# Optimization experiments

Measured on AMD Instinct MI355X. Metric: run time of the kernel, lower is better.

Reference implementation:

```python
import jax, jax.numpy as jnp
import numpy as np

# Supernet configuration (matches init_kwargs)
HIDDEN = [1024, 2048]
HEADS = [8, 16]
ABITS = [4, 8]
WBITS = [4, 8]
B, S = 4, 4096
MAX_IN = max(HIDDEN)            # 2048
MAX_OUT = max(HIDDEN)           # min(heads)*max(hidden)//min(heads) = 2048


def fake_quant(v, s, bit):
    """LSQ-style symmetric fake quantization with straight-through rounding."""
    qp = float(2 ** (bit - 1) - 1)
    qn = -float(2 ** (bit - 1))
    vs = jnp.clip(v / s, qn, qp)
    vq = vs + jax.lax.stop_gradient(jnp.round(vs) - vs)  # STE round
    return vq * s


def setup_inputs() -> dict:
    key = jax.random.key(0)
    k1, k2, k3, k4 = jax.random.split(key, 4)
    x = jax.random.normal(k1, (B, S, MAX_IN), jnp.float32)
    weights = jax.random.uniform(k2, (16,), jnp.float32)  # arch mixing coeffs
    W = jax.random.normal(k3, (MAX_OUT, MAX_IN), jnp.float32) * 0.02
    b = jax.random.normal(k4, (MAX_OUT,), jnp.float32) * 0.02
    # init_weight_scale: LSQ init 2*mean(|W|)/sqrt(Qp) per weight bitwidth
    w_scales = jnp.stack([2.0 * jnp.mean(jnp.abs(W)) / jnp.sqrt(float(2 ** (bit - 1) - 1))
                          for bit in WBITS])
    a_scales = jnp.ones((len(ABITS),), jnp.float32)
    return {"x": x, "weights": weights, "W": W, "b": b,
            "a_scales": a_scales, "w_scales": w_scales}


def reference(x, weights, W, b, a_scales, w_scales):
    # Non-argmax mixture path (reverse=False):
    # for each (hidden_i, heads_j, abit_m, wbit_n): slice W to
    # [out_dim, in_dim], zero-pad to [MAX_OUT, MAX_IN] (== masking, since
    # per-tensor fake-quant maps 0 -> 0), quantize, and weighted-accumulate.
    # Quantized x / W depend only on abit / wbit, so compute each once.
    qx = [fake_quant(x, a_scales[m], ABITS[m]) for m in range(len(ABITS))]   # [B,S,MAX_IN]
    qw = [fake_quant(W, w_scales[n], WBITS[n]) for n in range(len(WBITS))]  # [MAX_OUT,MAX_IN]
    out_idx = jnp.arange(MAX_OUT)
    in_idx = jnp.arange(MAX_IN)

    w_mix = jnp.zeros_like(W)
    x_mix = jnp.zeros_like(x)
    b_mix = jnp.zeros_like(b)
    k = 0
    for i, h in enumerate(HIDDEN):
        for j, nh in enumerate(HEADS):
            head_dim = h // nh
            out_dim = nh * head_dim  # == h when divisible
            in_dim = h
            wmask = (out_idx[:, None] < out_dim) & (in_idx[None, :] < in_dim)
            bmask = out_idx < out_dim
            for m in range(len(ABITS)):
                for n in range(len(WBITS)):
                    a = weights[k]
                    w_mix = w_mix + a * jnp.where(wmask, qw[n], 0.0)
                    x_mix = x_mix + a * qx[m]
                    b_mix = b_mix + a * jnp.where(bmask, b, 0.0)
                    k += 1
    # out = F.linear(x_mix, w_mix, b_mix)
    out = jnp.einsum('bsi,oi->bso', x_mix, w_mix) + b_mix
    return out
```

## Files before the change

### kernel.cpp

```cpp
#include <hip/hip_runtime.h>
#include <hip/hip_bf16.h>
#include <stdint.h>

#define MDIM 16384
#define NDIM 2048
#define KDIM 2048

typedef __attribute__((ext_vector_type(4))) float f32x4;
typedef __attribute__((ext_vector_type(8))) short s16x8;

__device__ __forceinline__ void gload_lds16(const __hip_bfloat16* g, void* l) {
    __builtin_amdgcn_global_load_lds(
        (const __attribute__((address_space(1))) void*)g,
        (__attribute__((address_space(3))) void*)l,
        16, 0, 0);
}


__global__ __launch_bounds__(256) void prep_x(
    const float* __restrict__ x, const float* __restrict__ weights,
    const float* __restrict__ a_scales, __hip_bfloat16* __restrict__ xq)
{
    float A0 = 0.f, A1 = 0.f;
    #pragma unroll
    for (int k = 0; k < 16; ++k) {
        float w = weights[k];
        if (((k >> 1) & 1) == 0) A0 += w; else A1 += w;
    }
    const float s0 = a_scales[0], s1 = a_scales[1];
    const float r0 = 1.f / s0, r1 = 1.f / s1;

    size_t idx = ((size_t)blockIdx.x * 256 + threadIdx.x) * 8;
    const f32x4* xv = (const f32x4*)(x + idx);
    f32x4 v0 = xv[0], v1 = xv[1];
    float vals[8] = {v0.x, v0.y, v0.z, v0.w, v1.x, v1.y, v1.z, v1.w};

    union { s16x8 v; __hip_bfloat16 h[8]; } u;
    #pragma unroll
    for (int j = 0; j < 8; ++j) {
        float q0 = rintf(fminf(fmaxf(vals[j] * r0, -8.f),   7.f)) * s0;
        float q1 = rintf(fminf(fmaxf(vals[j] * r1, -128.f), 127.f)) * s1;
        u.h[j] = __float2bfloat16(A0 * q0 + A1 * q1);
    }
    *(s16x8*)(xq + idx) = u.v;
}

__global__ __launch_bounds__(256) void prep_w(
    const float* __restrict__ W, const float* __restrict__ weights,
    const float* __restrict__ w_scales, __hip_bfloat16* __restrict__ wq)
{
    float c00 = weights[0] + weights[2]  + weights[4]  + weights[6];
    float c01 = weights[1] + weights[3]  + weights[5]  + weights[7];
    float c10 = weights[8] + weights[10] + weights[12] + weights[14];
    float c11 = weights[9] + weights[11] + weights[13] + weights[15];

    const float s0 = w_scales[0], s1 = w_scales[1];
    const float r0 = 1.f / s0, r1 = 1.f / s1;

    size_t idx = ((size_t)blockIdx.x * 256 + threadIdx.x) * 8;
    const int o = (int)(idx >> 11);
    const int c = (int)(idx & 2047);
    const bool inner = (o < 1024) && (c < 1024);
    const float k0 = inner ? (c00 + c10) : c10;
    const float k1 = inner ? (c01 + c11) : c11;

    const f32x4* wv = (const f32x4*)(W + idx);
    f32x4 v0 = wv[0], v1 = wv[1];
    float vals[8] = {v0.x, v0.y, v0.z, v0.w, v1.x, v1.y, v1.z, v1.w};

    union { s16x8 v; __hip_bfloat16 h[8]; } u;
    #pragma unroll
    for (int j = 0; j < 8; ++j) {
        float q0 = rintf(fminf(fmaxf(vals[j] * r0, -8.f),   7.f)) * s0;
        float q1 = rintf(fminf(fmaxf(vals[j] * r1, -128.f), 127.f)) * s1;
        u.h[j] = __float2bfloat16(k0 * q0 + k1 * q1);
    }
    *(s16x8*)(wq + idx) = u.v;
}

__global__ __launch_bounds__(256) void prep_b(
    const float* __restrict__ b, const float* __restrict__ weights,
    float* __restrict__ bm)
{
    int o = blockIdx.x * 256 + threadIdx.x;
    if (o >= NDIM) return;
    float S1 = 0.f, S0 = 0.f;
    #pragma unroll
    for (int k = 0; k < 8; ++k)  S0 += weights[k];
    #pragma unroll
    for (int k = 8; k < 16; ++k) S1 += weights[k];
    bm[o] = b[o] * ((o < 1024) ? (S0 + S1) : S1);
}


#define BM 256
#define BN 256
#define NCH 64
#define SLOTB 32768

#define MFMA(a, b, c) __builtin_amdgcn_mfma_f32_16x16x32_bf16((a), (b), (c), 0, 0, 0)

#define STEP(afU, bfU, afL, bfL, S1, S3)                                     \
  {                                                                          \
    gload_lds16(As0 + kg * 32, lds + (S3) * SLOTB + ldoff);                  \
    gload_lds16(As1 + kg * 32, lds + (S3) * SLOTB +  8192 + ldoff);          \
    _Pragma("unroll")                                                        \
    for (int m_ = 0; m_ < 8; ++m_)                                           \
      afL[m_] = *(const s16x8*)(lds + (S1) * SLOTB + aoff + m_ * 1024);      \
    asm volatile("s_waitcnt lgkmcnt(8)" ::: "memory");                       \
    __builtin_amdgcn_sched_barrier(0);                                       \
    __builtin_amdgcn_s_setprio(1);                                           \
    _Pragma("unroll")                                                        \
    for (int m_ = 0; m_ < 8; ++m_) {                                         \
      acc[m_][0] = MFMA(afU[m_], bfU[0], acc[m_][0]);                        \
      acc[m_][1] = MFMA(afU[m_], bfU[1], acc[m_][1]);                        \
    }                                                                        \
    __builtin_amdgcn_s_setprio(0);                                           \
    gload_lds16(Bs0 + kg * 32, lds + (S3) * SLOTB + 16384 + ldoff);          \
    gload_lds16(Bs1 + kg * 32, lds + (S3) * SLOTB + 24576 + ldoff);          \
    _Pragma("unroll")                                                        \
    for (int n_ = 0; n_ < 4; ++n_)                                           \
      bfL[n_] = *(const s16x8*)(lds + (S1) * SLOTB + 16384 + boff + n_ * 1024); \
    __builtin_amdgcn_s_setprio(1);                                           \
    _Pragma("unroll")                                                        \
    for (int m_ = 0; m_ < 8; ++m_) {                                         \
      acc[m_][2] = MFMA(afU[m_], bfU[2], acc[m_][2]);                        \
      acc[m_][3] = MFMA(afU[m_], bfU[3], acc[m_][3]);                        \
    }                                                                        \
    __builtin_amdgcn_s_setprio(0);                                           \
    kg = (kg + 1) & (NCH - 1);                                               \
    asm volatile("s_waitcnt vmcnt(4)" ::: "memory");                         \
    __builtin_amdgcn_s_barrier();                                            \
  }

__global__ __launch_bounds__(512, 2) void gemm256(
    const __hip_bfloat16* __restrict__ A,
    const __hip_bfloat16* __restrict__ B,
    const float* __restrict__ bias,
    float* __restrict__ C)
{
    __shared__ char lds[4 * SLOTB];

    const int tid  = threadIdx.x;
    const int lane = tid & 63;
    const int wid  = tid >> 6;
    const int wm   = wid >> 2;
    const int wn   = wid & 3;

    const int bid  = blockIdx.x;
    const int swz  = (bid & 7) * 64 + (bid >> 3);
    const int brow = (swz >> 3) * BM;
    const int bcol = (swz & 7) * BN;

    const int csw = (tid & 3) ^ ((tid >> 3) & 3);
    const __hip_bfloat16* As0 = A + (size_t)(brow + (tid >> 2)) * KDIM + csw * 8;
    const __hip_bfloat16* As1 = As0 + (size_t)128 * KDIM;
    const __hip_bfloat16* Bs0 = B + (size_t)(bcol + (tid >> 2)) * KDIM + csw * 8;
    const __hip_bfloat16* Bs1 = Bs0 + (size_t)128 * KDIM;
    const int ldoff = tid * 16;

    const int fr  = lane & 15;
    const int l16 = lane >> 4;
    const int xr  = (l16 ^ ((fr >> 1) & 3)) * 16;
    const int aoff = (wm * 128 + fr) * 64 + xr;
    const int boff = (wn * 64  + fr) * 64 + xr;

    f32x4 acc[8][4];
    #pragma unroll
    for (int m = 0; m < 8; ++m)
        #pragma unroll
        for (int n = 0; n < 4; ++n)
            acc[m][n] = (f32x4){0.f, 0.f, 0.f, 0.f};

    s16x8 af0[8], bf0[4], af1[8], bf1[4];
    int kg = 0;

    #pragma unroll
    for (int q = 0; q < 3; ++q) {
        gload_lds16(As0 + q * 32, lds + q * SLOTB + ldoff);
        gload_lds16(As1 + q * 32, lds + q * SLOTB +  8192 + ldoff);
        gload_lds16(Bs0 + q * 32, lds + q * SLOTB + 16384 + ldoff);
        gload_lds16(Bs1 + q * 32, lds + q * SLOTB + 24576 + ldoff);
    }
    kg = 3;
    asm volatile("s_waitcnt vmcnt(4)" ::: "memory");
    __builtin_amdgcn_s_barrier();
    #pragma unroll
    for (int m = 0; m < 8; ++m)
        af0[m] = *(const s16x8*)(lds + aoff + m * 1024);
    #pragma unroll
    for (int n = 0; n < 4; ++n)
        bf0[n] = *(const s16x8*)(lds + 16384 + boff + n * 1024);

    #pragma unroll 1
    for (int it = 0; it < NCH / 4; ++it) {
        STEP(af0, bf0, af1, bf1, 1, 3);
        STEP(af1, bf1, af0, bf0, 2, 0);
        STEP(af0, bf0, af1, bf1, 3, 1);
        STEP(af1, bf1, af0, bf0, 0, 2);
    }
    asm volatile("s_waitcnt vmcnt(0) lgkmcnt(0)" ::: "memory");

    const int ccol0 = bcol + wn * 64 + fr;
    const int crow0 = brow + wm * 128 + l16 * 4;
    float bv[4];
    #pragma unroll
    for (int n = 0; n < 4; ++n) bv[n] = bias[ccol0 + n * 16];

    #pragma unroll
    for (int m = 0; m < 8; ++m) {
        #pragma unroll
        for (int j = 0; j < 4; ++j) {
            float* Crow = C + (size_t)(crow0 + m * 16 + j) * NDIM;
            #pragma unroll
            for (int n = 0; n < 4; ++n)
                Crow[ccol0 + n * 16] = acc[m][n][j] + bv[n];
        }
    }
}


extern "C" void kernel_launch(void* const* d_in, const int* in_sizes, int n_in,
                              void* d_out, int out_size, void* d_ws, size_t ws_size,
                              hipStream_t stream) {
    const float* x        = (const float*)d_in[0];
    const float* weights  = (const float*)d_in[1];
    const float* W        = (const float*)d_in[2];
    const float* b        = (const float*)d_in[3];
    const float* a_scales = (const float*)d_in[4];
    const float* w_scales = (const float*)d_in[5];
    float* out = (float*)d_out;

    __hip_bfloat16* xq = (__hip_bfloat16*)d_ws;
    __hip_bfloat16* wq = (__hip_bfloat16*)((char*)d_ws + 67108864);
    float*          bm = (float*)((char*)d_ws + 67108864 + 8388608);

    prep_w<<<dim3((NDIM * KDIM) / (256 * 8)), dim3(256), 0, stream>>>(W, weights, w_scales, wq);
    prep_b<<<dim3(NDIM / 256), dim3(256), 0, stream>>>(b, weights, bm);
    prep_x<<<dim3(((size_t)MDIM * KDIM) / (256 * 8)), dim3(256), 0, stream>>>(x, weights, a_scales, xq);
    gemm256<<<dim3((MDIM / BM) * (NDIM / BN)), dim3(512), 0, stream>>>(xq, wq, bm, out);
}
```

Measured before the change: 161.3 us.

## Replace register double-buffered GEMM loop with split-phase LDS pipeline and barriers

Restructures the GEMM main loop. The register double buffering of A/B fragments (the next chunk's fragments loaded while the current chunk's MFMAs run) becomes a single fragment set read from LDS inside each chunk. Each chunk is split into two phases separated by workgroup barriers, and global-to-LDS prefetches are interleaved between them with a vmcnt(8) wait depth. This halves fragment register usage, which could help occupancy or scheduling, but it exposes LDS read latency before the MFMAs and adds three barriers per chunk.

```diff
diff --git a/kernel.cpp b/kernel.cpp
--- a/kernel.cpp
+++ b/kernel.cpp
@@ -100,37 +100,45 @@
 
 #define MFMA(a, b, c) __builtin_amdgcn_mfma_f32_16x16x32_bf16((a), (b), (c), 0, 0, 0)
 
-#define STEP(afU, bfU, afL, bfL, S1, S3)                                     \
+#define CHUNK(S, T)                                                          \
   {                                                                          \
-    gload_lds16(As0 + kg * 32, lds + (S3) * SLOTB + ldoff);                  \
-    gload_lds16(As1 + kg * 32, lds + (S3) * SLOTB +  8192 + ldoff);          \
+                                                      \
     _Pragma("unroll")                                                        \
     for (int m_ = 0; m_ < 8; ++m_)                                           \
-      afL[m_] = *(const s16x8*)(lds + (S1) * SLOTB + aoff + m_ * 1024);      \
-    asm volatile("s_waitcnt lgkmcnt(8)" ::: "memory");                       \
+      af[m_] = *(const s16x8*)(lds + (S) * SLOTB + aoff + m_ * 1024);        \
+    bf[0] = *(const s16x8*)(lds + (S) * SLOTB + 16384 + boff);               \
+    bf[1] = *(const s16x8*)(lds + (S) * SLOTB + 16384 + boff + 1024);        \
+    gload_lds16(As0 + kg * 32, lds + (T) * SLOTB + ldoff);                   \
+    gload_lds16(As1 + kg * 32, lds + (T) * SLOTB + 8192 + ldoff);            \
+    __builtin_amdgcn_s_barrier();                                            \
+    asm volatile("s_waitcnt lgkmcnt(0)" ::: "memory");                       \
     __builtin_amdgcn_sched_barrier(0);                                       \
     __builtin_amdgcn_s_setprio(1);                                           \
     _Pragma("unroll")                                                        \
     for (int m_ = 0; m_ < 8; ++m_) {                                         \
-      acc[m_][0] = MFMA(afU[m_], bfU[0], acc[m_][0]);                        \
-      acc[m_][1] = MFMA(afU[m_], bfU[1], acc[m_][1]);                        \
+      acc[m_][0] = MFMA(af[m_], bf[0], acc[m_][0]);                          \
+      acc[m_][1] = MFMA(af[m_], bf[1], acc[m_][1]);                          \
     }                                                                        \
     __builtin_amdgcn_s_setprio(0);                                           \
-    gload_lds16(Bs0 + kg * 32, lds + (S3) * SLOTB + 16384 + ldoff);          \
-    gload_lds16(Bs1 + kg * 32, lds + (S3) * SLOTB + 24576 + ldoff);          \
-    _Pragma("unroll")                                                        \
-    for (int n_ = 0; n_ < 4; ++n_)                                           \
-      bfL[n_] = *(const s16x8*)(lds + (S1) * SLOTB + 16384 + boff + n_ * 1024); \
+    __builtin_amdgcn_s_barrier();                                            \
+                                                      \
+    bf[2] = *(const s16x8*)(lds + (S) * SLOTB + 16384 + boff + 2048);        \
+    bf[3] = *(const s16x8*)(lds + (S) * SLOTB + 16384 + boff + 3072);        \
+    gload_lds16(Bs0 + kg * 32, lds + (T) * SLOTB + 16384 + ldoff);           \
+    gload_lds16(Bs1 + kg * 32, lds + (T) * SLOTB + 24576 + ldoff);           \
+    asm volatile("s_waitcnt vmcnt(8)" ::: "memory");                         \
+    __builtin_amdgcn_s_barrier();                                            \
+    asm volatile("s_waitcnt lgkmcnt(0)" ::: "memory");                       \
+    __builtin_amdgcn_sched_barrier(0);                                       \
     __builtin_amdgcn_s_setprio(1);                                           \
     _Pragma("unroll")                                                        \
     for (int m_ = 0; m_ < 8; ++m_) {                                         \
-      acc[m_][2] = MFMA(afU[m_], bfU[2], acc[m_][2]);                        \
-      acc[m_][3] = MFMA(afU[m_], bfU[3], acc[m_][3]);                        \
+      acc[m_][2] = MFMA(af[m_], bf[2], acc[m_][2]);                          \
+      acc[m_][3] = MFMA(af[m_], bf[3], acc[m_][3]);                          \
     }                                                                        \
     __builtin_amdgcn_s_setprio(0);                                           \
+    __builtin_amdgcn_s_barrier();                                            \
     kg = (kg + 1) & (NCH - 1);                                               \
-    asm volatile("s_waitcnt vmcnt(4)" ::: "memory");                         \
-    __builtin_amdgcn_s_barrier();                                            \
   }
 
 __global__ __launch_bounds__(512, 2) void gemm256(
@@ -172,8 +180,8 @@
         for (int n = 0; n < 4; ++n)
             acc[m][n] = (f32x4){0.f, 0.f, 0.f, 0.f};
 
-    s16x8 af0[8], bf0[4], af1[8], bf1[4];
-    int kg = 0;
+    s16x8 af[8], bf[4];
+    int kg = 3;
 
     #pragma unroll
     for (int q = 0; q < 3; ++q) {
@@ -182,22 +190,15 @@
         gload_lds16(Bs0 + q * 32, lds + q * SLOTB + 16384 + ldoff);
         gload_lds16(Bs1 + q * 32, lds + q * SLOTB + 24576 + ldoff);
     }
-    kg = 3;
-    asm volatile("s_waitcnt vmcnt(4)" ::: "memory");
+    asm volatile("s_waitcnt vmcnt(8)" ::: "memory");
     __builtin_amdgcn_s_barrier();
-    #pragma unroll
-    for (int m = 0; m < 8; ++m)
-        af0[m] = *(const s16x8*)(lds + aoff + m * 1024);
-    #pragma unroll
-    for (int n = 0; n < 4; ++n)
-        bf0[n] = *(const s16x8*)(lds + 16384 + boff + n * 1024);
 
     #pragma unroll 1
     for (int it = 0; it < NCH / 4; ++it) {
-        STEP(af0, bf0, af1, bf1, 1, 3);
-        STEP(af1, bf1, af0, bf0, 2, 0);
-        STEP(af0, bf0, af1, bf1, 3, 1);
-        STEP(af1, bf1, af0, bf0, 0, 2);
+        CHUNK(0, 3);
+        CHUNK(1, 0);
+        CHUNK(2, 1);
+        CHUNK(3, 2);
     }
     asm volatile("s_waitcnt vmcnt(0) lgkmcnt(0)" ::: "memory");
 
```

New measurement: 166.0 us. 1.03x slower.
